# Kernel optimization log

Hardware: AMD Instinct MI355X
Metric: run time of the kernel (lower is better)

The kernel has to match this reference:

```python
import jax, jax.numpy as jnp
import numpy as np

H = 4096      # hidden_size
NH = 32       # num_heads
QR = 1536     # q_lora_rank
KVR = 512     # kv_lora_rank
RD = 64       # qk_rope_head_dim
ND = 128      # qk_nope_head_dim
VD = 128      # v_head_dim
QK = RD + ND  # qk_head_dim
EPS = 1e-6
THETA = 10000.0
B, S = 2, 1024


def rmsnorm(x, w):
    # torch: x / (||x|| * d^-0.5 + eps) * w
    norm = jnp.sqrt(jnp.sum(x * x, axis=-1, keepdims=True)) * (x.shape[-1] ** -0.5)
    return x / (norm + EPS) * w


def rope_cos_sin(seq_len):
    inv_freq = 1.0 / (THETA ** (jnp.arange(0, RD, 2, dtype=jnp.float32) / RD))
    t = jnp.arange(seq_len, dtype=jnp.float32)
    freqs = jnp.outer(t, inv_freq)              # [S, RD/2]
    emb = jnp.concatenate([freqs, freqs], -1)   # [S, RD]
    return jnp.cos(emb), jnpp_cos_sin_dummy() if False else jnp.sin(emb)


def rotate_half(x):
    x1, x2 = jnp.split(x, 2, axis=-1)
    return jnp.concatenate([-x2, x1], axis=-1)


def setup_inputs() -> dict:
    key = jax.random.key(0)
    ks = jax.random.split(key, 8)
    sc = 0.02
    return {
        "hidden_states": jax.random.normal(ks[0], (B, S, H), jnp.float32),
        "w_qa": jax.random.normal(ks[1], (H, QR), jnp.float32) * sc,
        "g_qa": jnp.ones((QR,), jnp.float32),
        "w_qb": jax.random.normal(ks[2], (QR, NH * QK), jnp.float32) * sc,
        "w_kva": jax.random.normal(ks[3], (H, KVR + RD), jnp.float32) * sc,
        "g_kva": jnp.ones((KVR,), jnp.float32),
        "w_kvb": jax.random.normal(ks[4], (KVR, NH * (ND + VD)), jnp.float32) * sc,
        "w_o": jax.random.normal(ks[5], (NH * VD, H), jnp.float32) * sc,
    }


def reference(hidden_states, w_qa, g_qa, w_qb, w_kva, g_kva, w_kvb, w_o):
    b, s, _ = hidden_states.shape
    # Q path: LoRA down -> RMSNorm -> LoRA up
    q_c = rmsnorm(hidden_states @ w_qa, g_qa)                       # [b,s,QR]
    q = (q_c @ w_qb).reshape(b, s, NH, QK).transpose(0, 2, 1, 3)    # [b,NH,s,QK]
    q_nope, q_rope = q[..., :ND], q[..., ND:]
    # KV path: joint down-proj, split compressed kv and rope key
    kv = hidden_states @ w_kva                                      # [b,s,KVR+RD]
    k_c, k_rope = kv[..., :KVR], kv[..., KVR:]
    k_c = rmsnorm(k_c, g_kva)
    kst = (k_c @ w_kvb).reshape(b, s, NH, ND + VD).transpose(0, 2, 1, 3)
    k_nope, v = kst[..., :ND], kst[..., ND:]                        # [b,NH,s,ND],[b,NH,s,VD]
    # partial RoPE on the rope slice only
    inv_freq = 1.0 / (THETA ** (jnp.arange(0, RD, 2, dtype=jnp.float32) / RD))
    freqs = jnp.outer(jnp.arange(s, dtype=jnp.float32), inv_freq)
    emb = jnp.concatenate([freqs, freqs], -1)                       # [s,RD]
    cos = jnp.cos(emb)[None, None]                                  # [1,1,s,RD]
    sin = jnp.sin(emb)[None, None]
    k_rope = k_rope[:, None]                                        # [b,1,s,RD]
    q_rope = q_rope * cos + rotate_half(q_rope) * sin
    k_rope = k_rope * cos + rotate_half(k_rope) * sin
    k_rope = jnp.broadcast_to(k_rope, (b, NH, s, RD))
    query = jnp.concatenate([q_nope, q_rope], -1)                   # [b,NH,s,QK]
    key_s = jnp.concatenate([k_nope, k_rope], -1)
    scaling = QK ** -0.5
    scores = jnp.einsum("bhqd,bhkd->bhqk", query, key_s) * scaling  # [b,NH,s,s]
    attn = jax.nn.softmax(scores, axis=-1)
    out = jnp.einsum("bhqk,bhkd->bhqd", attn, v)                    # [b,NH,s,VD]
    out = out.transpose(0, 2, 1, 3).reshape(b, s, NH * VD)
    return out @ w_o                                                # [b,s,H]
```

## Files before the change

### kernel.cpp

```cpp
#include <hip/hip_runtime.h>
#include <hip/hip_bf16.h>
#include <stdint.h>

typedef float f32x4_t __attribute__((ext_vector_type(4)));
typedef short s16x8_t __attribute__((ext_vector_type(8)));

#define LDS_AS __attribute__((address_space(3)))
#define GLB_AS __attribute__((address_space(1)))

__device__ __forceinline__ void gload16(void* lds, const void* g) {
    __builtin_amdgcn_global_load_lds((const GLB_AS uint32_t*)g,
                                     (LDS_AS uint32_t*)lds, 16, 0, 0);
}

__global__ __launch_bounds__(256) void rope_table_kernel(float* __restrict__ cos_t,
                                                         float* __restrict__ sin_t) {
    int idx = blockIdx.x * 256 + threadIdx.x;
    int s = idx >> 6, j = idx & 63;
    float invf = powf(10000.0f, -((float)((j & 31) * 2)) / 64.0f);
    float a = (float)s * invf;
    cos_t[idx] = cosf(a);
    sin_t[idx] = sinf(a);
}

__global__ __launch_bounds__(256) void f32_to_bf16_kernel(const float* __restrict__ in,
                                                          __hip_bfloat16* __restrict__ out, int n4) {
    int i = blockIdx.x * 256 + threadIdx.x;
    if (i >= n4) return;
    float4 v = reinterpret_cast<const float4*>(in)[i];
    struct __align__(8) BF4 { __hip_bfloat16 a, b, c, d; } r;
    r.a = __float2bfloat16(v.x); r.b = __float2bfloat16(v.y);
    r.c = __float2bfloat16(v.z); r.d = __float2bfloat16(v.w);
    reinterpret_cast<BF4*>(out)[i] = r;
}

__global__ __launch_bounds__(256) void transpose_convert(const float* __restrict__ W,
                                                         __hip_bfloat16* __restrict__ WT,
                                                         int K, int N, int Npad, float scale) {
    __shared__ float tile[32][33];
    int k0 = blockIdx.y * 32, n0 = blockIdx.x * 32;
    int tx = threadIdx.x & 31, ty = threadIdx.x >> 5;
#pragma unroll
    for (int i = 0; i < 4; i++) {
        int ky = i * 8 + ty;
        int n = n0 + tx;
        float v = 0.f;
        if (n < N) v = W[(size_t)(k0 + ky) * N + n];
        tile[ky][tx] = v;
    }
    __syncthreads();
#pragma unroll
    for (int i = 0; i < 4; i++) {
        int ny = i * 8 + ty;
        WT[(size_t)(n0 + ny) * K + k0 + tx] = __float2bfloat16(tile[tx][ny] * scale);
    }
}

__global__ __launch_bounds__(256) void rmsnorm_kernel(const float* __restrict__ in,
                                                      const float* __restrict__ g,
                                                      __hip_bfloat16* __restrict__ out,
                                                      int cols, int in_stride) {
    int row = blockIdx.x;
    const float* x = in + (size_t)row * in_stride;
    float ss = 0.f;
    for (int c = threadIdx.x; c < cols; c += 256) { float v = x[c]; ss += v * v; }
#pragma unroll
    for (int off = 32; off > 0; off >>= 1) ss += __shfl_xor(ss, off);
    __shared__ float red[4];
    if ((threadIdx.x & 63) == 0) red[threadIdx.x >> 6] = ss;
    __syncthreads();
    float tot = red[0] + red[1] + red[2] + red[3];
    float rms = sqrtf(tot / (float)cols);
    float inv = 1.0f / (rms + 1e-6f);
    for (int c = threadIdx.x; c < cols; c += 256)
        out[(size_t)row * cols + c] = __float2bfloat16(x[c] * inv * g[c]);
}

__global__ __launch_bounds__(256) void rope_k_kernel(const float* __restrict__ kv,
                                                     const float* __restrict__ cos_t,
                                                     const float* __restrict__ sin_t,
                                                     __hip_bfloat16* __restrict__ k_rope) {
    int idx = blockIdx.x * 256 + threadIdx.x;
    int tok = idx >> 5, j = idx & 31;
    int s = tok & 1023;
    const float* x = kv + (size_t)tok * 640 + 512;
    float x1 = x[j], x2 = x[j + 32];
    float co = cos_t[s * 64 + j], si = sin_t[s * 64 + j];
    __hip_bfloat16* o = k_rope + (size_t)tok * 64;
    o[j]      = __float2bfloat16(x1 * co - x2 * si);
    o[j + 32] = __float2bfloat16(x2 * co + x1 * si);
}

__global__ __launch_bounds__(256) void rope_q_kernel(__hip_bfloat16* __restrict__ q,
                                                     const float* __restrict__ cos_t,
                                                     const float* __restrict__ sin_t) {
    int tok = blockIdx.x;
    int s = tok & 1023;
    __hip_bfloat16* row = q + (size_t)tok * 6144;
#pragma unroll
    for (int it = 0; it < 4; it++) {
        int i = it * 256 + threadIdx.x;
        int h = i >> 5, j = i & 31;
        int c = h * 192 + 128 + j;
        float x1 = __bfloat162float(row[c]), x2 = __bfloat162float(row[c + 32]);
        float co = cos_t[s * 64 + j], si = sin_t[s * 64 + j];
        row[c]      = __float2bfloat16(x1 * co - x2 * si);
        row[c + 32] = __float2bfloat16(x2 * co + x1 * si);
    }
}

__global__ __launch_bounds__(256) void transpose_v_kernel(const __hip_bfloat16* __restrict__ kst,
                                                          __hip_bfloat16* __restrict__ V_T) {
    __shared__ __hip_bfloat16 t[64][136];
    int bid = blockIdx.x;
    int st = bid & 15, bh = bid >> 4;
    int h = bh & 31, b = bh >> 5;
    int s0 = st * 64;
#pragma unroll
    for (int i = 0; i < 4; i++) {
        int c = i * 256 + threadIdx.x;
        int r = c >> 4, oct = c & 15;
        *(s16x8_t*)&t[r][oct * 8] =
            *(const s16x8_t*)&kst[(size_t)(b * 1024 + s0 + r) * 8192 + h * 256 + 128 + oct * 8];
    }
    __syncthreads();
#pragma unroll
    for (int i = 0; i < 4; i++) {
        int c = i * 256 + threadIdx.x;
        int vd = c >> 3, oct = c & 7;
        s16x8_t pk;
#pragma unroll
        for (int e = 0; e < 8; e++) pk[e] = *(const short*)&t[oct * 8 + e][vd];
        *(s16x8_t*)&V_T[((size_t)bh * 128 + vd) * 1024 + s0 + oct * 8] = pk;
    }
}

template <int MODE>
__global__ __launch_bounds__(256, 2) void gemm_bt_128(const __hip_bfloat16* __restrict__ A,
                                                      const __hip_bfloat16* __restrict__ BT,
                                                      void* __restrict__ Cout, void* __restrict__ C1,
                                                      int M, int N, int K, int N0, int N1) {
    __shared__ __hip_bfloat16 As[128 * 64];
    __shared__ __hip_bfloat16 Bs[128 * 64];
    const int tid = threadIdx.x;
    const int l = tid & 63, w = tid >> 6;
    const int wr = w >> 1, wc = w & 1;
    const int m0 = blockIdx.y * 128, n0 = blockIdx.x * 128;
    const int lrow = l & 15, lkg = l >> 4;

    f32x4_t acc[4][4];
#pragma unroll
    for (int i = 0; i < 4; i++)
#pragma unroll
        for (int j = 0; j < 4; j++) acc[i][j] = (f32x4_t){0.f, 0.f, 0.f, 0.f};

    for (int k0 = 0; k0 < K; k0 += 64) {
        __syncthreads();
#pragma unroll
        for (int i = 0; i < 4; i++) {
            int s = i * 256 + tid;
            int row = s >> 3, po = s & 7;
            int lo = po ^ (row & 7);
            gload16(&As[s * 8], &A[(size_t)(m0 + row) * K + k0 + lo * 8]);
            gload16(&Bs[s * 8], &BT[(size_t)(n0 + row) * K + k0 + lo * 8]);
        }
        __syncthreads();
#pragma unroll
        for (int ks = 0; ks < 2; ks++) {
            s16x8_t a[4], b[4];
#pragma unroll
            for (int m = 0; m < 4; m++) {
                int row = wr * 64 + m * 16 + lrow;
                int oct = (ks * 4 + lkg) ^ (row & 7);
                a[m] = *(const s16x8_t*)&As[row * 64 + oct * 8];
            }
#pragma unroll
            for (int n = 0; n < 4; n++) {
                int row = wc * 64 + n * 16 + lrow;
                int oct = (ks * 4 + lkg) ^ (row & 7);
                b[n] = *(const s16x8_t*)&Bs[row * 64 + oct * 8];
            }
#pragma unroll
            for (int m = 0; m < 4; m++)
#pragma unroll
                for (int n = 0; n < 4; n++)
                    acc[m][n] = __builtin_amdgcn_mfma_f32_16x16x32_bf16(a[m], b[n], acc[m][n], 0, 0, 0);
        }
    }
#pragma unroll
    for (int m = 0; m < 4; m++) {
        int row = m0 + wr * 64 + m * 16 + lkg * 4;
#pragma unroll
        for (int n = 0; n < 4; n++) {
            int col = n0 + wc * 64 + n * 16 + lrow;
#pragma unroll
            for (int r = 0; r < 4; r++) {
                float v = acc[m][n][r];
                if (MODE == 1) {
                    ((__hip_bfloat16*)Cout)[(size_t)(row + r) * N + col] = __float2bfloat16(v);
                } else if (MODE == 0) {
                    ((float*)Cout)[(size_t)(row + r) * N + col] = v;
                } else {
                    if (col < N0) ((float*)Cout)[(size_t)(row + r) * N0 + col] = v;
                    else          ((float*)C1)[(size_t)(row + r) * N1 + (col - N0)] = v;
                }
            }
        }
    }
}

__global__ __launch_bounds__(256, 2) void attn7_kernel(const __hip_bfloat16* __restrict__ q,
                                                       const __hip_bfloat16* __restrict__ kst,
                                                       const __hip_bfloat16* __restrict__ k_rope,
                                                       const __hip_bfloat16* __restrict__ V_T,
                                                       __hip_bfloat16* __restrict__ attn_out) {
    __shared__ __align__(16) __hip_bfloat16 Ks[2][64 * 192];
    __shared__ __align__(16) __hip_bfloat16 Ps[64 * 72];

    int i = blockIdx.x;
    int bh = (i & 7) * 8 + ((i >> 3) & 7);
    int qt = i >> 6;
    int h = bh & 31, b = bh >> 5;
    int q0 = qt * 64;
    int tid = threadIdx.x, l = tid & 63, w = tid >> 6;
    int lrow = l & 15, lkg = l >> 4;

    s16x8_t qa[6];
    {
        size_t qbase = (size_t)(b * 1024 + q0 + w * 16 + lrow) * 6144 + h * 192;
#pragma unroll
        for (int f = 0; f < 6; f++)
            qa[f] = *(const s16x8_t*)&q[qbase + f * 32 + lkg * 8];
    }
    f32x4_t acc_o[8];
#pragma unroll
    for (int n = 0; n < 8; n++) acc_o[n] = (f32x4_t){0.f, 0.f, 0.f, 0.f};
    float m_run[4] = {-1e30f, -1e30f, -1e30f, -1e30f};
    float l_run[4] = {0.f, 0.f, 0.f, 0.f};

    size_t krow_base = (size_t)(b * 1024) * 8192 + h * 256;
    size_t rrow_base = (size_t)(b * 1024) * 64;
    const __hip_bfloat16* vbase = V_T + (size_t)bh * 128 * 1024 + (size_t)lrow * 1024 + lkg * 8;

    auto stage_k = [&](int kv0, int buf) {
#pragma unroll
        for (int it = 0; it < 6; it++) {
            int s = it * 256 + tid;
            int row = s / 24, po = s - row * 24;
            int lo = po ^ (row & 7);
            const __hip_bfloat16* src = (lo < 16)
                ? &kst[krow_base + (size_t)(kv0 + row) * 8192 + lo * 8]
                : &k_rope[rrow_base + (size_t)(kv0 + row) * 64 + (lo - 16) * 8];
            gload16(&Ks[buf][s * 8], src);
        }
    };

    stage_k(0, 0);
    asm volatile("s_waitcnt vmcnt(0)" ::: "memory");
    __syncthreads();

    int cur = 0;
    for (int kt = 0; kt < 16; kt++) {
        int kv0 = kt * 64;

        if (kt < 15) stage_k(kv0 + 64, cur ^ 1);

        f32x4_t sc[4];
#pragma unroll
        for (int c = 0; c < 4; c++) sc[c] = (f32x4_t){0.f, 0.f, 0.f, 0.f};
        __builtin_amdgcn_s_setprio(1);
#pragma unroll
        for (int c = 0; c < 4; c++) {
            int row = c * 16 + lrow;
#pragma unroll
            for (int f = 0; f < 6; f++) {
                int po = ((f * 4 + lkg) ^ (lrow & 7)) * 8;
                s16x8_t kb = *(const s16x8_t*)&Ks[cur][row * 192 + po];
                sc[c] = __builtin_amdgcn_mfma_f32_16x16x32_bf16(qa[f], kb, sc[c], 0, 0, 0);
            }
        }
        __builtin_amdgcn_s_setprio(0);

        s16x8_t vb0[8], vb1[8];
#pragma unroll
        for (int n = 0; n < 8; n++)
            vb0[n] = *(const s16x8_t*)&vbase[(size_t)(n * 16) * 1024 + kv0];
#pragma unroll
        for (int n = 0; n < 8; n++)
            vb1[n] = *(const s16x8_t*)&vbase[(size_t)(n * 16) * 1024 + kv0 + 32];
        __builtin_amdgcn_sched_barrier(0);

        float mx[4];
#pragma unroll
        for (int r = 0; r < 4; r++) {
            float m0 = fmaxf(fmaxf(sc[0][r], sc[1][r]), fmaxf(sc[2][r], sc[3][r]));
#pragma unroll
            for (int off = 1; off < 16; off <<= 1) m0 = fmaxf(m0, __shfl_xor(m0, off));
            mx[r] = m0;
        }
        int small = (mx[0] - m_run[0] <= 8.0f) && (mx[1] - m_run[1] <= 8.0f) &&
                    (mx[2] - m_run[2] <= 8.0f) && (mx[3] - m_run[3] <= 8.0f);
        if (!__all(small)) {
#pragma unroll
            for (int r = 0; r < 4; r++) {
                float mn = fmaxf(m_run[r], mx[r]);
                float al = __expf(m_run[r] - mn);
                m_run[r] = mn;
                l_run[r] *= al;
#pragma unroll
                for (int n = 0; n < 8; n++) acc_o[n][r] *= al;
            }
        }
#pragma unroll
        for (int r = 0; r < 4; r++) {
            float sum = 0.f;
            float p[4];
#pragma unroll
            for (int c = 0; c < 4; c++) {
                p[c] = __expf(sc[c][r] - m_run[r]);
                sum += p[c];
            }
#pragma unroll
            for (int c = 0; c < 4; c++)
                Ps[(w * 16 + lkg * 4 + r) * 72 + c * 16 + lrow] = __float2bfloat16(p[c]);
#pragma unroll
            for (int off = 1; off < 16; off <<= 1) sum += __shfl_xor(sum, off);
            l_run[r] += sum;
        }
        asm volatile("s_waitcnt lgkmcnt(0)" ::: "memory");
        __builtin_amdgcn_sched_barrier(0);

        __builtin_amdgcn_s_setprio(1);
        {
            s16x8_t pa = *(const s16x8_t*)&Ps[(w * 16 + lrow) * 72 + lkg * 8];
#pragma unroll
            for (int n = 0; n < 8; n++)
                acc_o[n] = __builtin_amdgcn_mfma_f32_16x16x32_bf16(pa, vb0[n], acc_o[n], 0, 0, 0);
        }
        {
            s16x8_t pa = *(const s16x8_t*)&Ps[(w * 16 + lrow) * 72 + 32 + lkg * 8];
#pragma unroll
            for (int n = 0; n < 8; n++)
                acc_o[n] = __builtin_amdgcn_mfma_f32_16x16x32_bf16(pa, vb1[n], acc_o[n], 0, 0, 0);
        }
        __builtin_amdgcn_s_setprio(0);

        asm volatile("s_waitcnt vmcnt(0)" ::: "memory");
        __syncthreads();
        cur ^= 1;
    }
#pragma unroll
    for (int r = 0; r < 4; r++) {
        float inv = 1.0f / l_run[r];
        size_t tok = (size_t)(b * 1024 + q0 + w * 16 + lkg * 4 + r);
#pragma unroll
        for (int n = 0; n < 8; n++)
            attn_out[tok * 4096 + h * 128 + n * 16 + lrow] =
                __float2bfloat16(acc_o[n][r] * inv);
    }
}

extern "C" void kernel_launch(void* const* d_in, const int* in_sizes, int n_in,
                              void* d_out, int out_size, void* d_ws, size_t ws_size,
                              hipStream_t stream) {
    const float* hidden = (const float*)d_in[0];
    const float* w_qa   = (const float*)d_in[1];
    const float* g_qa   = (const float*)d_in[2];
    const float* w_qb   = (const float*)d_in[3];
    const float* w_kva  = (const float*)d_in[4];
    const float* g_kva  = (const float*)d_in[5];
    const float* w_kvb  = (const float*)d_in[6];
    const float* w_o    = (const float*)d_in[7];
    float* out = (float*)d_out;

    char* base = (char*)d_ws;
    size_t off = 0;
    auto alloc = [&](size_t bytes) -> void* {
        off = (off + 255) & ~(size_t)255;
        void* p = base + off;
        off += bytes;
        return p;
    };
    float* cos_t = (float*)alloc(1024 * 64 * 4);
    float* sin_t = (float*)alloc(1024 * 64 * 4);
    __hip_bfloat16* hid_b  = (__hip_bfloat16*)alloc(2048ull * 4096 * 2);
    __hip_bfloat16* wqaT   = (__hip_bfloat16*)alloc(1536ull * 4096 * 2);
    __hip_bfloat16* wkvaT  = (__hip_bfloat16*)alloc(640ull * 4096 * 2);
    __hip_bfloat16* wqbT   = (__hip_bfloat16*)alloc(6144ull * 1536 * 2);
    __hip_bfloat16* wkvbT  = (__hip_bfloat16*)alloc(8192ull * 512 * 2);
    __hip_bfloat16* woT    = (__hip_bfloat16*)alloc(4096ull * 4096 * 2);
    float* q_a             = (float*)alloc(2048ull * 1536 * 4);
    __hip_bfloat16* q_c    = (__hip_bfloat16*)alloc(2048ull * 1536 * 2);
    __hip_bfloat16* q_buf  = (__hip_bfloat16*)alloc(2048ull * 6144 * 2);
    float* kv              = (float*)alloc(2048ull * 640 * 4);
    __hip_bfloat16* k_c    = (__hip_bfloat16*)alloc(2048ull * 512 * 2);
    __hip_bfloat16* k_rope = (__hip_bfloat16*)alloc(2048ull * 64 * 2);
    __hip_bfloat16* kst    = (__hip_bfloat16*)alloc(2048ull * 8192 * 2);
    __hip_bfloat16* V_T      = hid_b;
    __hip_bfloat16* attn_out = wqbT;

    const float qscale = 0.07216878364870323f;

    rope_table_kernel<<<256, 256, 0, stream>>>(cos_t, sin_t);
    f32_to_bf16_kernel<<<8192, 256, 0, stream>>>(hidden, hid_b, 2048 * 4096 / 4);
    transpose_convert<<<dim3(1536 / 32, 4096 / 32), 256, 0, stream>>>(w_qa, wqaT, 4096, 1536, 1536, 1.0f);
    transpose_convert<<<dim3(640 / 32, 4096 / 32), 256, 0, stream>>>(w_kva, wkvaT, 4096, 576, 640, 1.0f);
    transpose_convert<<<dim3(6144 / 32, 1536 / 32), 256, 0, stream>>>(w_qb, wqbT, 1536, 6144, 6144, qscale);
    transpose_convert<<<dim3(8192 / 32, 512 / 32), 256, 0, stream>>>(w_kvb, wkvbT, 512, 8192, 8192, 1.0f);
    transpose_convert<<<dim3(4096 / 32, 4096 / 32), 256, 0, stream>>>(w_o, woT, 4096, 4096, 4096, 1.0f);

    gemm_bt_128<2><<<dim3(17, 16), 256, 0, stream>>>(hid_b, wqaT, q_a, kv, 2048, 2176, 4096, 1536, 640);
    rmsnorm_kernel<<<2048, 256, 0, stream>>>(q_a, g_qa, q_c, 1536, 1536);
    rmsnorm_kernel<<<2048, 256, 0, stream>>>(kv, g_kva, k_c, 512, 640);
    rope_k_kernel<<<2048 * 32 / 256, 256, 0, stream>>>(kv, cos_t, sin_t, k_rope);
    gemm_bt_128<1><<<dim3(6144 / 128, 16), 256, 0, stream>>>(q_c, wqbT, q_buf, nullptr, 2048, 6144, 1536, 0, 0);
    rope_q_kernel<<<2048, 256, 0, stream>>>(q_buf, cos_t, sin_t);
    gemm_bt_128<1><<<dim3(8192 / 128, 16), 256, 0, stream>>>(k_c, wkvbT, kst, nullptr, 2048, 8192, 512, 0, 0);
    transpose_v_kernel<<<1024, 256, 0, stream>>>(kst, V_T);
    attn7_kernel<<<1024, 256, 0, stream>>>(q_buf, kst, k_rope, V_T, attn_out);
    gemm_bt_128<0><<<dim3(4096 / 128, 16), 256, 0, stream>>>(attn_out, woT, out, nullptr, 2048, 4096, 4096, 0, 0);
}
```

Baseline: 475.4 us.

## Transpose attention MFMA so softmax rows stay in-lane and P is passed via shuffles

Swaps the MFMA operand order in QK^T and PV so each lane holds one query row's scores. This lets max and sum reductions use two cross-lane shuffles instead of four, and keeps a single scalar running max and sum per lane. The P tile moves from an LDS round trip to register shuffles, which removes its shared buffer and the wait before PV. V loads are split into halves to lower register pressure so launch bounds can be raised to three blocks per SM, and the output is staged through LDS for 16-byte coalesced stores. The risks are extra shuffle and select instructions and whether the occupancy target actually fits in the available registers.

```diff
diff --git a/kernel.cpp b/kernel.cpp
--- a/kernel.cpp
+++ b/kernel.cpp
@@ -1,6 +1,7 @@
 #include <hip/hip_runtime.h>
 #include <hip/hip_bf16.h>
 #include <stdint.h>
+#include <string.h>
 
 typedef float f32x4_t __attribute__((ext_vector_type(4)));
 typedef short s16x8_t __attribute__((ext_vector_type(8)));
@@ -11,6 +12,12 @@
 __device__ __forceinline__ void gload16(void* lds, const void* g) {
     __builtin_amdgcn_global_load_lds((const GLB_AS uint32_t*)g,
                                      (LDS_AS uint32_t*)lds, 16, 0, 0);
+}
+
+__device__ __forceinline__ uint32_t pack_bf16(float lo, float hi) {
+    union { __hip_bfloat16 h; uint16_t u; } a, b;
+    a.h = __float2bfloat16(lo); b.h = __float2bfloat16(hi);
+    return (uint32_t)a.u | ((uint32_t)b.u << 16);
 }
 
 __global__ __launch_bounds__(256) void rope_table_kernel(float* __restrict__ cos_t,
@@ -209,13 +216,12 @@
     }
 }
 
-__global__ __launch_bounds__(256, 2) void attn7_kernel(const __hip_bfloat16* __restrict__ q,
+__global__ __launch_bounds__(256, 3) void attn8_kernel(const __hip_bfloat16* __restrict__ q,
                                                        const __hip_bfloat16* __restrict__ kst,
                                                        const __hip_bfloat16* __restrict__ k_rope,
                                                        const __hip_bfloat16* __restrict__ V_T,
                                                        __hip_bfloat16* __restrict__ attn_out) {
     __shared__ __align__(16) __hip_bfloat16 Ks[2][64 * 192];
-    __shared__ __align__(16) __hip_bfloat16 Ps[64 * 72];
 
     int i = blockIdx.x;
     int bh = (i & 7) * 8 + ((i >> 3) & 7);
@@ -235,8 +241,7 @@
     f32x4_t acc_o[8];
 #pragma unroll
     for (int n = 0; n < 8; n++) acc_o[n] = (f32x4_t){0.f, 0.f, 0.f, 0.f};
-    float m_run[4] = {-1e30f, -1e30f, -1e30f, -1e30f};
-    float l_run[4] = {0.f, 0.f, 0.f, 0.f};
+    float m_run = -1e30f, l_run = 0.f;
 
     size_t krow_base = (size_t)(b * 1024) * 8192 + h * 256;
     size_t rrow_base = (size_t)(b * 1024) * 64;
@@ -259,6 +264,10 @@
     asm volatile("s_waitcnt vmcnt(0)" ::: "memory");
     __syncthreads();
 
+    const int src0 = lrow + ((lkg & 1) << 5);
+    const int src1 = src0 + 16;
+    const bool hiC = (lkg >> 1) != 0;
+
     int cur = 0;
     for (int kt = 0; kt < 16; kt++) {
         int kv0 = kt * 64;
@@ -276,87 +285,105 @@
             for (int f = 0; f < 6; f++) {
                 int po = ((f * 4 + lkg) ^ (lrow & 7)) * 8;
                 s16x8_t kb = *(const s16x8_t*)&Ks[cur][row * 192 + po];
-                sc[c] = __builtin_amdgcn_mfma_f32_16x16x32_bf16(qa[f], kb, sc[c], 0, 0, 0);
+                sc[c] = __builtin_amdgcn_mfma_f32_16x16x32_bf16(kb, qa[f], sc[c], 0, 0, 0);
             }
         }
         __builtin_amdgcn_s_setprio(0);
 
-        s16x8_t vb0[8], vb1[8];
+        s16x8_t vb0[8];
 #pragma unroll
         for (int n = 0; n < 8; n++)
             vb0[n] = *(const s16x8_t*)&vbase[(size_t)(n * 16) * 1024 + kv0];
+        __builtin_amdgcn_sched_barrier(0);
+
+        float mx = sc[0][0];
+#pragma unroll
+        for (int c = 0; c < 4; c++)
+#pragma unroll
+            for (int r = 0; r < 4; r++) mx = fmaxf(mx, sc[c][r]);
+        mx = fmaxf(mx, __shfl_xor(mx, 16));
+        mx = fmaxf(mx, __shfl_xor(mx, 32));
+        if (!__all(mx - m_run <= 8.0f)) {
+            float mn = fmaxf(m_run, mx);
+            float al = __expf(m_run - mn);
+            m_run = mn;
+            l_run *= al;
+#pragma unroll
+            for (int n = 0; n < 8; n++) acc_o[n] *= al;
+        }
+        uint32_t u[4][2];
+        float sum = 0.f;
+#pragma unroll
+        for (int c = 0; c < 4; c++) {
+            float p0 = __expf(sc[c][0] - m_run), p1 = __expf(sc[c][1] - m_run);
+            float p2 = __expf(sc[c][2] - m_run), p3 = __expf(sc[c][3] - m_run);
+            sum += (p0 + p1) + (p2 + p3);
+            u[c][0] = pack_bf16(p0, p1);
+            u[c][1] = pack_bf16(p2, p3);
+        }
+        sum += __shfl_xor(sum, 16);
+        sum += __shfl_xor(sum, 32);
+        l_run += sum;
+
+        {
+            uint32_t a0 = __shfl((int)u[0][0], src0), b0 = __shfl((int)u[1][0], src0);
+            uint32_t a1 = __shfl((int)u[0][1], src0), b1 = __shfl((int)u[1][1], src0);
+            uint32_t a2 = __shfl((int)u[0][0], src1), b2 = __shfl((int)u[1][0], src1);
+            uint32_t a3 = __shfl((int)u[0][1], src1), b3 = __shfl((int)u[1][1], src1);
+            union { uint32_t wd[4]; s16x8_t v; } pb;
+            pb.wd[0] = hiC ? b0 : a0;
+            pb.wd[1] = hiC ? b1 : a1;
+            pb.wd[2] = hiC ? b2 : a2;
+            pb.wd[3] = hiC ? b3 : a3;
+            __builtin_amdgcn_s_setprio(1);
+#pragma unroll
+            for (int n = 0; n < 8; n++)
+                acc_o[n] = __builtin_amdgcn_mfma_f32_16x16x32_bf16(vb0[n], pb.v, acc_o[n], 0, 0, 0);
+            __builtin_amdgcn_s_setprio(0);
+        }
+        s16x8_t vb1[8];
 #pragma unroll
         for (int n = 0; n < 8; n++)
             vb1[n] = *(const s16x8_t*)&vbase[(size_t)(n * 16) * 1024 + kv0 + 32];
-        __builtin_amdgcn_sched_barrier(0);
-
-        float mx[4];
-#pragma unroll
-        for (int r = 0; r < 4; r++) {
-            float m0 = fmaxf(fmaxf(sc[0][r], sc[1][r]), fmaxf(sc[2][r], sc[3][r]));
-#pragma unroll
-            for (int off = 1; off < 16; off <<= 1) m0 = fmaxf(m0, __shfl_xor(m0, off));
-            mx[r] = m0;
-        }
-        int small = (mx[0] - m_run[0] <= 8.0f) && (mx[1] - m_run[1] <= 8.0f) &&
-                    (mx[2] - m_run[2] <= 8.0f) && (mx[3] - m_run[3] <= 8.0f);
-        if (!__all(small)) {
-#pragma unroll
-            for (int r = 0; r < 4; r++) {
-                float mn = fmaxf(m_run[r], mx[r]);
-                float al = __expf(m_run[r] - mn);
-                m_run[r] = mn;
-                l_run[r] *= al;
-#pragma unroll
-                for (int n = 0; n < 8; n++) acc_o[n][r] *= al;
-            }
-        }
-#pragma unroll
-        for (int r = 0; r < 4; r++) {
-            float sum = 0.f;
-            float p[4];
-#pragma unroll
-            for (int c = 0; c < 4; c++) {
-                p[c] = __expf(sc[c][r] - m_run[r]);
-                sum += p[c];
-            }
-#pragma unroll
-            for (int c = 0; c < 4; c++)
-                Ps[(w * 16 + lkg * 4 + r) * 72 + c * 16 + lrow] = __float2bfloat16(p[c]);
-#pragma unroll
-            for (int off = 1; off < 16; off <<= 1) sum += __shfl_xor(sum, off);
-            l_run[r] += sum;
-        }
-        asm volatile("s_waitcnt lgkmcnt(0)" ::: "memory");
-        __builtin_amdgcn_sched_barrier(0);
-
-        __builtin_amdgcn_s_setprio(1);
         {
-            s16x8_t pa = *(const s16x8_t*)&Ps[(w * 16 + lrow) * 72 + lkg * 8];
+            uint32_t a0 = __shfl((int)u[2][0], src0), b0 = __shfl((int)u[3][0], src0);
+            uint32_t a1 = __shfl((int)u[2][1], src0), b1 = __shfl((int)u[3][1], src0);
+            uint32_t a2 = __shfl((int)u[2][0], src1), b2 = __shfl((int)u[3][0], src1);
+            uint32_t a3 = __shfl((int)u[2][1], src1), b3 = __shfl((int)u[3][1], src1);
+            union { uint32_t wd[4]; s16x8_t v; } pb;
+            pb.wd[0] = hiC ? b0 : a0;
+            pb.wd[1] = hiC ? b1 : a1;
+            pb.wd[2] = hiC ? b2 : a2;
+            pb.wd[3] = hiC ? b3 : a3;
+            __builtin_amdgcn_s_setprio(1);
 #pragma unroll
             for (int n = 0; n < 8; n++)
-                acc_o[n] = __builtin_amdgcn_mfma_f32_16x16x32_bf16(pa, vb0[n], acc_o[n], 0, 0, 0);
-        }
-        {
-            s16x8_t pa = *(const s16x8_t*)&Ps[(w * 16 + lrow) * 72 + 32 + lkg * 8];
-#pragma unroll
-            for (int n = 0; n < 8; n++)
-                acc_o[n] = __builtin_amdgcn_mfma_f32_16x16x32_bf16(pa, vb1[n], acc_o[n], 0, 0, 0);
-        }
-        __builtin_amdgcn_s_setprio(0);
+                acc_o[n] = __builtin_amdgcn_mfma_f32_16x16x32_bf16(vb1[n], pb.v, acc_o[n], 0, 0, 0);
+            __builtin_amdgcn_s_setprio(0);
+        }
 
         asm volatile("s_waitcnt vmcnt(0)" ::: "memory");
         __syncthreads();
         cur ^= 1;
     }
-#pragma unroll
-    for (int r = 0; r < 4; r++) {
-        float inv = 1.0f / l_run[r];
-        size_t tok = (size_t)(b * 1024 + q0 + w * 16 + lkg * 4 + r);
-#pragma unroll
-        for (int n = 0; n < 8; n++)
-            attn_out[tok * 4096 + h * 128 + n * 16 + lrow] =
-                __float2bfloat16(acc_o[n][r] * inv);
+
+    float inv = 1.0f / l_run;
+    __hip_bfloat16* Ob = &Ks[0][0] + (size_t)w * (16 * 136);
+#pragma unroll
+    for (int n = 0; n < 8; n++) {
+        uint32_t lo = pack_bf16(acc_o[n][0] * inv, acc_o[n][1] * inv);
+        uint32_t hi = pack_bf16(acc_o[n][2] * inv, acc_o[n][3] * inv);
+        uint32_t* dst = (uint32_t*)&Ob[lrow * 136 + n * 16 + lkg * 4];
+        dst[0] = lo;
+        dst[1] = hi;
+    }
+    asm volatile("s_waitcnt lgkmcnt(0)" ::: "memory");
+    __builtin_amdgcn_sched_barrier(0);
+#pragma unroll
+    for (int it = 0; it < 4; it++) {
+        int tr = it * 4 + lkg;
+        s16x8_t ov = *(const s16x8_t*)&Ob[tr * 136 + lrow * 8];
+        *(s16x8_t*)&attn_out[(size_t)(b * 1024 + q0 + w * 16 + tr) * 4096 + h * 128 + lrow * 8] = ov;
     }
 }
 
@@ -417,6 +444,6 @@
     rope_q_kernel<<<2048, 256, 0, stream>>>(q_buf, cos_t, sin_t);
     gemm_bt_128<1><<<dim3(8192 / 128, 16), 256, 0, stream>>>(k_c, wkvbT, kst, nullptr, 2048, 8192, 512, 0, 0);
     transpose_v_kernel<<<1024, 256, 0, stream>>>(kst, V_T);
-    attn7_kernel<<<1024, 256, 0, stream>>>(q_buf, kst, k_rope, V_T, attn_out);
+    attn8_kernel<<<1024, 256, 0, stream>>>(q_buf, kst, k_rope, V_T, attn_out);
     gemm_bt_128<0><<<dim3(4096 / 128, 16), 256, 0, stream>>>(attn_out, woT, out, nullptr, 2048, 4096, 4096, 0, 0);
 }
```

New measurement: 465.9 us. 2.0% less time.
